# Optimization experiments

Measured on AMD Instinct MI355X. Metric: run time of the kernel, lower is better.

The kernel has to match this reference:

```python
import jax, jax.numpy as jnp
import numpy as np

NU, NI, F, H, D = 100000, 50000, 256, 8, 64
E1, E2 = 300000, 300000
SLOPE = 0.2  # DGL GATConv default negative_slope


def setup_inputs() -> dict:
    key = jax.random.key(0)
    ks = jax.random.split(key, 20)
    p = lambda k, sh: jax.random.normal(k, sh, jnp.float32) * 0.1
    return {
        "h_user": jax.random.normal(ks[0], (NU, F), jnp.float32),
        "h_item": jax.random.normal(ks[1], (NI, F), jnp.float32),
        "src_u2i": jax.random.randint(ks[2], (E1,), 0, NU),
        "dst_u2i": jax.random.randint(ks[3], (E1,), 0, NI),
        "src_i2u": jax.random.randint(ks[4], (E2,), 0, NI),
        "dst_i2u": jax.random.randint(ks[5], (E2,), 0, NU),
        "W_src_u2i": p(ks[6], (F, H * D)), "W_dst_u2i": p(ks[7], (F, H * D)),
        "al_u2i": p(ks[8], (H, D)), "ar_u2i": p(ks[9], (H, D)),
        "bias_u2i": jnp.zeros((H * D,), jnp.float32), "W_res_u2i": p(ks[10], (F, H * D)),
        "W_src_i2u": p(ks[11], (F, H * D)), "W_dst_i2u": p(ks[12], (F, H * D)),
        "al_i2u": p(ks[13], (H, D)), "ar_i2u": p(ks[14], (H, D)),
        "bias_i2u": jnp.zeros((H * D,), jnp.float32), "W_res_i2u": p(ks[15], (F, H * D)),
    }


def _gat(h_src, h_dst, src, dst, Ws, Wd, al, ar, b, Wr, n_dst):
    # linear projections -> [N, H, D]
    fs = (h_src @ Ws).reshape(-1, H, D)
    fd = (h_dst @ Wd).reshape(-1, H, D)
    el = jnp.einsum('nhd,hd->nh', fs, al)   # a_l . Wh_src
    er = jnp.einsum('nhd,hd->nh', fd, ar)   # a_r . Wh_dst
    e = jax.nn.leaky_relu(el[src] + er[dst], SLOPE)  # [E, H]
    # segment softmax over incoming edges of each dst node
    m = jax.ops.segment_max(e, dst, num_segments=n_dst)
    m = jnp.where(jnp.isfinite(m), m, jnp.float32(0))  # nodes with no edges
    ex = jnp.exp(e - m[dst])
    s = jax.ops.segment_sum(ex, dst, num_segments=n_dst)
    a = ex / s[dst]                                   # [E, H]
    # weighted scatter-sum of gathered source features
    out = jax.ops.segment_sum(a[:, :, None] * fs[src], dst, num_segments=n_dst)
    res = (h_dst @ Wr).reshape(-1, H, D)              # residual projection
    return out + res + b.reshape(1, H, D)


def reference(h_user, h_item, src_u2i, dst_u2i, src_i2u, dst_i2u,
              W_src_u2i, W_dst_u2i, al_u2i, ar_u2i, bias_u2i, W_res_u2i,
              W_src_i2u, W_dst_i2u, al_i2u, ar_i2u, bias_i2u, W_res_i2u):
    out_item = _gat(h_user, h_item, src_u2i, dst_u2i,
                    W_src_u2i, W_dst_u2i, al_u2i, ar_u2i, bias_u2i, W_res_u2i, NI)
    out_user = _gat(h_item, h_user, src_i2u, dst_i2u,
                    W_src_i2u, W_dst_i2u, al_i2u, ar_i2u, bias_i2u, W_res_i2u, NU)
    return (out_user, out_item)
```

## Files before the change

kernel.cpp:

```cpp
#include <hip/hip_runtime.h>
#include <cstdint>
#include <cstddef>

#define NU_ 100000
#define NI_ 50000
#define F_ 256
#define H_ 8
#define HD_ 512
#define NE_ 300000
#define SLOPE_ 0.2f

#define MPAD_U 100096
#define MPAD_I 50048
#define MT_U (MPAD_U / 128)
#define MT_I (MPAD_I / 128)
#define GEMM_NB ((MT_U + MT_I) * 4)

#define SCAN_N (NI_ + NU_)
#define SCAN_CHUNK 2048
#define SCAN_NB ((SCAN_N + SCAN_CHUNK - 1) / SCAN_CHUNK)

#define PREP_COPY_U (NU_ * F_ / 2048)
#define PREP_COPY_I (NI_ * F_ / 2048)
#define PREP_COPY (PREP_COPY_U + PREP_COPY_I)
#define PREP_WCONV 2048
#define PREP_FOLD 32
#define PREP_HIST ((2 * NE_ + 255) / 256)
#define PREP_NB (PREP_COPY + PREP_WCONV + PREP_FOLD + PREP_HIST)

typedef float f32x4 __attribute__((ext_vector_type(4)));
typedef __bf16 bf16x8 __attribute__((ext_vector_type(8)));
typedef unsigned short u16x8 __attribute__((ext_vector_type(8)));
typedef unsigned short u16x4 __attribute__((ext_vector_type(4)));

static __device__ __forceinline__ unsigned short f2bf_bits(float f) {
  unsigned u = __float_as_uint(f);
  u += 0x7fffu + ((u >> 16) & 1u);
  return (unsigned short)(u >> 16);
}
static __device__ __forceinline__ float bf2f(unsigned short b) {
  return __uint_as_float(((unsigned)b) << 16);
}

#define GLL16(g, l)                                                        \
  __builtin_amdgcn_global_load_lds(                                        \
      (const __attribute__((address_space(1))) void*)(g),                  \
      (__attribute__((address_space(3))) void*)(l), 16, 0, 0)

__global__ __launch_bounds__(256) void prep_kernel(const float* __restrict__ h_user,
                                                   const float* __restrict__ h_item,
                                                   const float* __restrict__ W0,
                                                   const float* __restrict__ W1,
                                                   const float* __restrict__ W2,
                                                   const float* __restrict__ W3,
                                                   const float* __restrict__ Wd0,
                                                   const float* __restrict__ Wd1,
                                                   const float* __restrict__ a0,
                                                   const float* __restrict__ a1,
                                                   const float* __restrict__ a2,
                                                   const float* __restrict__ a3,
                                                   const int* __restrict__ dst_u2i,
                                                   const int* __restrict__ dst_i2u,
                                                   unsigned short* __restrict__ hb_user,
                                                   unsigned short* __restrict__ hb_item,
                                                   unsigned short* __restrict__ Wt,
                                                   unsigned short* __restrict__ wfb,
                                                   int* __restrict__ deg) {
  int bid = blockIdx.x;
  if (bid < PREP_COPY) {
    bool user = bid < PREP_COPY_U;
    const float* h = user ? h_user : h_item;
    unsigned short* hb = user ? hb_user : hb_item;
    size_t base = (size_t)(user ? bid : bid - PREP_COPY_U) * 2048 + threadIdx.x * 8;
    f32x4 a = *(const f32x4*)&h[base];
    f32x4 b = *(const f32x4*)&h[base + 4];
    u16x8 o;
    o[0] = f2bf_bits(a.x); o[1] = f2bf_bits(a.y); o[2] = f2bf_bits(a.z); o[3] = f2bf_bits(a.w);
    o[4] = f2bf_bits(b.x); o[5] = f2bf_bits(b.y); o[6] = f2bf_bits(b.z); o[7] = f2bf_bits(b.w);
    *(u16x8*)&hb[base] = o;
  } else if (bid < PREP_COPY + PREP_WCONV) {
    int idx = (bid - PREP_COPY) * 256 + threadIdx.x;
    int m = idx >> 17;
    int r = idx & 131071;
    const float* W = (m == 0) ? W0 : (m == 1) ? W1 : (m == 2) ? W2 : W3;
    int f = r & 255, c = r >> 8;
    Wt[idx] = f2bf_bits(W[(size_t)f * HD_ + c]);
  } else if (bid < PREP_COPY + PREP_WCONV + PREP_FOLD) {
    int b = bid - PREP_COPY - PREP_WCONV;
    int m = b >> 3;
    int idx = (b & 7) * 256 + threadIdx.x;
    const float* W = (m == 0) ? W0 : (m == 1) ? Wd0 : (m == 2) ? W2 : Wd1;
    const float* av = (m == 0) ? a0 : (m == 1) ? a1 : (m == 2) ? a2 : a3;
    int f = idx & 255, hh = idx >> 8;
    float acc = 0.f;
#pragma unroll 8
    for (int d = 0; d < 64; ++d) acc += W[(size_t)f * HD_ + hh * 64 + d] * av[hh * 64 + d];
    int buf = (m == 0 || m == 3) ? 0 : 1;
    int rowoff = (m == 1 || m == 3) ? 8 : 0;
    wfb[buf * 4096 + (rowoff + hh) * 256 + f] = f2bf_bits(acc);
  } else {
    int e = (bid - PREP_COPY - PREP_WCONV - PREP_FOLD) * 256 + threadIdx.x;
    if (e < NE_) atomicAdd(&deg[dst_u2i[e]], 1);
    else if (e < 2 * NE_) atomicAdd(&deg[NI_ + dst_i2u[e - NE_]], 1);
  }
}

__global__ __launch_bounds__(256) void gemm2_kernel(const unsigned short* __restrict__ hb_user,
                                                    const unsigned short* __restrict__ hb_item,
                                                    const unsigned short* __restrict__ Wt,
                                                    const unsigned short* __restrict__ wfb,
                                                    unsigned short* __restrict__ fs_u2i,
                                                    unsigned short* __restrict__ fs_i2u,
                                                    unsigned short* __restrict__ res_user,
                                                    unsigned short* __restrict__ res_item,
                                                    const float* __restrict__ bias_u2i,
                                                    const float* __restrict__ bias_i2u,
                                                    float* __restrict__ el_u2i,
                                                    float* __restrict__ er_i2u,
                                                    float* __restrict__ el_i2u,
                                                    float* __restrict__ er_u2i,
                                                    const int* __restrict__ deg,
                                                    int* __restrict__ bsum) {
  __shared__ unsigned short lds[2][3][128][32];
  __shared__ unsigned short wflds[2][16][32];
  if (blockIdx.x >= GEMM_NB) {
    int* ilds = (int*)&lds[0][0][0][0];
    int tid = threadIdx.x;
    int base = (blockIdx.x - GEMM_NB) * SCAN_CHUNK + tid * 8;
    int sum = 0;
#pragma unroll
    for (int j = 0; j < 8; ++j) sum += (base + j < SCAN_N) ? deg[base + j] : 0;
    ilds[tid] = sum;
    __syncthreads();
    for (int o = 128; o > 0; o >>= 1) {
      if (tid < o) ilds[tid] += ilds[tid + o];
      __syncthreads();
    }
    if (tid == 0) bsum[blockIdx.x - GEMM_NB] = ilds[0];
    return;
  }
  int bid;
  {
    constexpr int qq = GEMM_NB / 8, rr = GEMM_NB % 8;
    int xcd = blockIdx.x & 7, sidx = blockIdx.x >> 3;
    bid = (xcd < rr ? xcd * (qq + 1) : rr * (qq + 1) + (xcd - rr) * qq) + sidx;
  }
  bool user = bid < MT_U * 4;
  if (!user) bid -= MT_U * 4;
  const unsigned short* Ab  = user ? hb_user : hb_item;
  const unsigned short* B1t = user ? (Wt + 0 * HD_ * F_) : (Wt + 2 * HD_ * F_);
  const unsigned short* B2t = user ? (Wt + 3 * HD_ * F_) : (Wt + 1 * HD_ * F_);
  const unsigned short* wfs = user ? wfb : (wfb + 4096);
  unsigned short* fs  = user ? fs_u2i : fs_i2u;
  unsigned short* res = user ? res_user : res_item;
  const float* bias = user ? bias_i2u : bias_u2i;
  int M = user ? NU_ : NI_;

  int tid = threadIdx.x;
  int lane = tid & 63;
  int wave = tid >> 6;
  int wm = wave >> 1, wn = wave & 1;
  int mt = bid >> 2, nt = bid & 3;
  int bm = mt * 128, bn = nt * 128;
  f32x4 acc1[4][4] = {};
  f32x4 acc2[4][4] = {};
  f32x4 acc3[4] = {};
  int lr = lane & 15;
  int ksw = ((lane >> 4) ^ ((lr >> 1) & 3)) << 3;

  int r0 = tid >> 2;
  int c0 = (tid & 3) << 3;
  int cs = (((tid & 3) ^ ((r0 >> 1) & 3)) << 3);
  const unsigned short* gA  = &Ab [(size_t)(bm + r0) * 256 + cs];
  const unsigned short* gB1 = &B1t[(size_t)(bn + r0) * 256 + cs];
  const unsigned short* gB2 = &B2t[(size_t)(bn + r0) * 256 + cs];
  const unsigned short* gW  = &wfs[(size_t)(tid >> 2) * 256 + cs];

#define STAGE(buf, t)                                                       \
  do {                                                                      \
    int k0_ = (t) * 32;                                                     \
    GLL16(gA  + k0_,          &lds[buf][0][r0][c0]);                        \
    GLL16(gA  + k0_ + 64*256, &lds[buf][0][r0 + 64][c0]);                   \
    GLL16(gB1 + k0_,          &lds[buf][1][r0][c0]);                        \
    GLL16(gB1 + k0_ + 64*256, &lds[buf][1][r0 + 64][c0]);                   \
    GLL16(gB2 + k0_,          &lds[buf][2][r0][c0]);                        \
    GLL16(gB2 + k0_ + 64*256, &lds[buf][2][r0 + 64][c0]);                   \
    if (nt == 0 && tid < 64) GLL16(gW + k0_, &wflds[buf][tid >> 2][c0]);    \
  } while (0)

  STAGE(0, 0);
#pragma unroll
  for (int t = 0; t < 8; ++t) {
    if (t < 7) STAGE((t + 1) & 1, t + 1);
    if (t < 7) asm volatile("s_waitcnt vmcnt(6)" ::: "memory");
    else       asm volatile("s_waitcnt vmcnt(0)" ::: "memory");
    __builtin_amdgcn_s_barrier();
    __builtin_amdgcn_sched_barrier(0);
    const int cb = t & 1;
    bf16x8 af[4], b1[4], b2[4];
#pragma unroll
    for (int m = 0; m < 4; ++m)
      af[m] = __builtin_bit_cast(bf16x8, *(const u16x8*)&lds[cb][0][wm * 64 + m * 16 + lr][ksw]);
#pragma unroll
    for (int n = 0; n < 4; ++n) {
      b1[n] = __builtin_bit_cast(bf16x8, *(const u16x8*)&lds[cb][1][wn * 64 + n * 16 + lr][ksw]);
      b2[n] = __builtin_bit_cast(bf16x8, *(const u16x8*)&lds[cb][2][wn * 64 + n * 16 + lr][ksw]);
    }
#pragma unroll
    for (int m = 0; m < 4; ++m)
#pragma unroll
      for (int n = 0; n < 4; ++n) {
        acc1[m][n] = __builtin_amdgcn_mfma_f32_16x16x32_bf16(af[m], b1[n], acc1[m][n], 0, 0, 0);
        acc2[m][n] = __builtin_amdgcn_mfma_f32_16x16x32_bf16(af[m], b2[n], acc2[m][n], 0, 0, 0);
      }
    if (nt == 0) {
      bf16x8 b3 = __builtin_bit_cast(bf16x8, *(const u16x8*)&wflds[cb][lr][ksw]);
#pragma unroll
      for (int m = 0; m < 4; ++m)
        acc3[m] = __builtin_amdgcn_mfma_f32_16x16x32_bf16(af[m], b3, acc3[m], 0, 0, 0);
    }
    __builtin_amdgcn_sched_barrier(0);
    __builtin_amdgcn_s_barrier();
  }
#undef STAGE

  int rg = (lane >> 4) * 4;
#pragma unroll
  for (int m = 0; m < 4; ++m) {
#pragma unroll
    for (int r = 0; r < 4; ++r) {
      int row = bm + wm * 64 + m * 16 + rg + r;
      if (row >= M) continue;
#pragma unroll
      for (int n = 0; n < 4; ++n) {
        int col = bn + wn * 64 + n * 16 + lr;
        fs[(size_t)row * HD_ + col]  = f2bf_bits(acc1[m][n][r]);
        res[(size_t)row * HD_ + col] = f2bf_bits(acc2[m][n][r] + bias[col]);
      }
    }
  }
  if (nt == 0 && wn == 0) {
    float* elp = user ? el_u2i : el_i2u;
    float* erp = user ? er_i2u : er_u2i;
#pragma unroll
    for (int m = 0; m < 4; ++m) {
#pragma unroll
      for (int r = 0; r < 4; ++r) {
        int row = bm + wm * 64 + m * 16 + rg + r;
        if (row >= M) continue;
        if (lr < 8) elp[(size_t)row * 8 + lr] = acc3[m][r];
        else        erp[(size_t)row * 8 + lr - 8] = acc3[m][r];
      }
    }
  }
}

__global__ __launch_bounds__(256) void scan_apply_kernel(const int* __restrict__ deg,
                                                         const int* __restrict__ bsum,
                                                         int* __restrict__ rowstart,
                                                         int* __restrict__ cursor) {
  __shared__ int sb[128];
  __shared__ int lds[256];
  int tid = threadIdx.x;
  if (tid < 128) sb[tid] = (tid < SCAN_NB) ? bsum[tid] : 0;
  __syncthreads();
  for (int o = 1; o < 128; o <<= 1) {
    int t = (tid < 128 && tid >= o) ? sb[tid - o] : 0;
    __syncthreads();
    if (tid < 128) sb[tid] += t;
    __syncthreads();
  }
  int blockpref = (blockIdx.x == 0) ? 0 : sb[blockIdx.x - 1];
  int base = blockIdx.x * SCAN_CHUNK + tid * 8;
  int v[8];
  int sum = 0;
#pragma unroll
  for (int j = 0; j < 8; ++j) {
    v[j] = (base + j < SCAN_N) ? deg[base + j] : 0;
    sum += v[j];
  }
  lds[tid] = sum;
  __syncthreads();
  for (int o = 1; o < 256; o <<= 1) {
    int t = (tid >= o) ? lds[tid - o] : 0;
    __syncthreads();
    lds[tid] += t;
    __syncthreads();
  }
  int run = blockpref + lds[tid] - sum;
#pragma unroll
  for (int j = 0; j < 8; ++j) {
    if (base + j < SCAN_N) { rowstart[base + j] = run; cursor[base + j] = run; }
    run += v[j];
  }
  if (blockIdx.x == 0 && tid == 0) rowstart[SCAN_N] = 2 * NE_;
}

__global__ __launch_bounds__(256) void bin_kernel(const int* __restrict__ src_u2i,
                                                  const int* __restrict__ dst_u2i,
                                                  const int* __restrict__ src_i2u,
                                                  const int* __restrict__ dst_i2u,
                                                  int* __restrict__ cursor,
                                                  int* __restrict__ ssrc) {
  int e = blockIdx.x * 256 + threadIdx.x;
  int de, se;
  if (e < NE_) { de = dst_u2i[e]; se = src_u2i[e]; }
  else if (e < 2 * NE_) { de = NI_ + dst_i2u[e - NE_]; se = src_i2u[e - NE_]; }
  else return;
  int pos = atomicAdd(&cursor[de], 1);
  ssrc[pos] = se;
}

__global__ __launch_bounds__(256) void accum_kernel(const int* __restrict__ rowstart,
                                                    const int* __restrict__ ssrc,
                                                    const float* __restrict__ el_u2i,
                                                    const float* __restrict__ el_i2u,
                                                    const float* __restrict__ er_u2i,
                                                    const float* __restrict__ er_i2u,
                                                    const unsigned short* __restrict__ fs_u2i,
                                                    const unsigned short* __restrict__ fs_i2u,
                                                    const unsigned short* __restrict__ res_user,
                                                    const unsigned short* __restrict__ res_item,
                                                    float* __restrict__ out_item,
                                                    float* __restrict__ out_user) {
  int n = blockIdx.x * 4 + (threadIdx.x >> 6);
  int lane = threadIdx.x & 63;
  bool item = n < NI_;
  int ln = item ? n : n - NI_;
  const unsigned short* res = item ? res_item : res_user;
  float* out = (item ? out_item : out_user) + (size_t)ln * HD_;
  int r0 = rowstart[n], r1 = rowstart[n + 1];
  float acc[8] = {};
  if (r0 < r1) {
    const float* el = item ? el_u2i : el_i2u;
    const float* er = item ? er_u2i : er_i2u;
    const unsigned short* fs = item ? fs_u2i : fs_i2u;
    int hh = lane >> 3;
    float erh = er[(size_t)ln * 8 + hh];
    float m = -3.0e38f, s = 0.f;
    int k = r0;
    for (; k + 2 <= r1; k += 2) {
      int s0 = ssrc[k], s1 = ssrc[k + 1];
      float e0 = el[(size_t)s0 * 8 + hh] + erh;
      float e1 = el[(size_t)s1 * 8 + hh] + erh;
      e0 = e0 > 0.f ? e0 : SLOPE_ * e0;
      e1 = e1 > 0.f ? e1 : SLOPE_ * e1;
      u16x8 v0 = *(const u16x8*)&fs[(size_t)s0 * HD_ + lane * 8];
      u16x8 v1 = *(const u16x8*)&fs[(size_t)s1 * HD_ + lane * 8];
      float mm = fmaxf(e0, e1);
      if (mm > m) {
        float r = __expf(m - mm);
        s *= r;
#pragma unroll
        for (int j = 0; j < 8; ++j) acc[j] *= r;
        m = mm;
      }
      float x0 = __expf(e0 - m), x1 = __expf(e1 - m);
      s += x0 + x1;
#pragma unroll
      for (int j = 0; j < 8; ++j)
        acc[j] += x0 * bf2f((unsigned short)v0[j]) + x1 * bf2f((unsigned short)v1[j]);
    }
    if (k < r1) {
      int s0 = ssrc[k];
      float e0 = el[(size_t)s0 * 8 + hh] + erh;
      e0 = e0 > 0.f ? e0 : SLOPE_ * e0;
      u16x8 v0 = *(const u16x8*)&fs[(size_t)s0 * HD_ + lane * 8];
      if (e0 > m) {
        float r = __expf(m - e0);
        s *= r;
#pragma unroll
        for (int j = 0; j < 8; ++j) acc[j] *= r;
        m = e0;
      }
      float x0 = __expf(e0 - m);
      s += x0;
#pragma unroll
      for (int j = 0; j < 8; ++j) acc[j] += x0 * bf2f((unsigned short)v0[j]);
    }
    float inv = 1.f / s;
#pragma unroll
    for (int j = 0; j < 8; ++j) acc[j] *= inv;
  }
  u16x8 rv = *(const u16x8*)&res[(size_t)ln * HD_ + lane * 8];
  f32x4 o0, o1;
#pragma unroll
  for (int j = 0; j < 4; ++j) {
    o0[j] = acc[j] + bf2f((unsigned short)rv[j]);
    o1[j] = acc[4 + j] + bf2f((unsigned short)rv[4 + j]);
  }
  float* op = out + lane * 8;
  *(f32x4*)op = o0;
  *(f32x4*)(op + 4) = o1;
}

extern "C" void kernel_launch(void* const* d_in, const int* in_sizes, int n_in,
                              void* d_out, int out_size, void* d_ws, size_t ws_size,
                              hipStream_t stream) {
  const float* h_user    = (const float*)d_in[0];
  const float* h_item    = (const float*)d_in[1];
  const int*   src_u2i   = (const int*)d_in[2];
  const int*   dst_u2i   = (const int*)d_in[3];
  const int*   src_i2u   = (const int*)d_in[4];
  const int*   dst_i2u   = (const int*)d_in[5];
  const float* W_src_u2i = (const float*)d_in[6];
  const float* W_dst_u2i = (const float*)d_in[7];
  const float* al_u2i    = (const float*)d_in[8];
  const float* ar_u2i    = (const float*)d_in[9];
  const float* bias_u2i  = (const float*)d_in[10];
  const float* W_res_u2i = (const float*)d_in[11];
  const float* W_src_i2u = (const float*)d_in[12];
  const float* W_dst_i2u = (const float*)d_in[13];
  const float* al_i2u    = (const float*)d_in[14];
  const float* ar_i2u    = (const float*)d_in[15];
  const float* bias_i2u  = (const float*)d_in[16];
  const float* W_res_i2u = (const float*)d_in[17];

  float* out_user = (float*)d_out;
  float* out_item = (float*)d_out + (size_t)NU_ * HD_;

  char* ws = (char*)d_ws;
  size_t off = 0;
  auto take = [&](size_t bytes) -> char* {
    char* p = ws + off;
    off += (bytes + 255) & ~(size_t)255;
    return p;
  };
  unsigned short* fs_u2i   = (unsigned short*)take((size_t)NU_ * HD_ * 2);
  unsigned short* fs_i2u   = (unsigned short*)take((size_t)NI_ * HD_ * 2);
  unsigned short* res_user = (unsigned short*)take((size_t)NU_ * HD_ * 2);
  unsigned short* res_item = (unsigned short*)take((size_t)NI_ * HD_ * 2);
  unsigned short* hb_user  = (unsigned short*)take((size_t)MPAD_U * F_ * 2);
  unsigned short* hb_item  = (unsigned short*)take((size_t)MPAD_I * F_ * 2);
  unsigned short* Wt  = (unsigned short*)take((size_t)4 * HD_ * F_ * 2);
  unsigned short* wfb = (unsigned short*)take((size_t)2 * 16 * F_ * 2);
  float* el_u2i = (float*)take((size_t)NU_ * 8 * 4);
  float* er_i2u = (float*)take((size_t)NU_ * 8 * 4);
  float* el_i2u = (float*)take((size_t)NI_ * 8 * 4);
  float* er_u2i = (float*)take((size_t)NI_ * 8 * 4);
  int* deg_all      = (int*)take((size_t)SCAN_N * 4);
  int* rowstart_all = (int*)take((size_t)(SCAN_N + 1) * 4);
  int* cursor_all   = (int*)take((size_t)SCAN_N * 4);
  int* bsum         = (int*)take((size_t)128 * 4);
  int* ssrc         = (int*)take((size_t)2 * NE_ * 4);

  hipMemsetAsync(deg_all, 0, (size_t)SCAN_N * 4, stream);

  prep_kernel<<<PREP_NB, 256, 0, stream>>>(h_user, h_item,
                                           W_src_u2i, W_res_u2i, W_src_i2u, W_res_i2u,
                                           W_dst_u2i, W_dst_i2u,
                                           al_u2i, ar_u2i, al_i2u, ar_i2u,
                                           dst_u2i, dst_i2u,
                                           hb_user, hb_item, Wt, wfb, deg_all);

  gemm2_kernel<<<GEMM_NB + SCAN_NB, 256, 0, stream>>>(hb_user, hb_item, Wt, wfb,
                                                      fs_u2i, fs_i2u, res_user, res_item,
                                                      bias_u2i, bias_i2u,
                                                      el_u2i, er_i2u, el_i2u, er_u2i,
                                                      deg_all, bsum);

  scan_apply_kernel<<<SCAN_NB, 256, 0, stream>>>(deg_all, bsum, rowstart_all, cursor_all);
  constexpr int EB2 = (2 * NE_ + 255) / 256;
  bin_kernel<<<EB2, 256, 0, stream>>>(src_u2i, dst_u2i, src_i2u, dst_i2u, cursor_all, ssrc);

  accum_kernel<<<SCAN_N / 4, 256, 0, stream>>>(rowstart_all, ssrc,
                                               el_u2i, el_i2u, er_u2i, er_i2u,
                                               fs_u2i, fs_i2u, res_user, res_item,
                                               out_item, out_user);
}
```

Before: 502.0 us.

## Load GEMM operands directly from global memory instead of LDS double-buffering

Removes the global_load_lds double-buffered staging and barriers in the fused projection GEMM. Each wave now loads its MFMA A/B fragments straight from global memory (bf16x8 per lane), relying on L1/L2 for reuse. Launch bounds now request two blocks per SM. This removes LDS traffic and synchronisation, but operands shared across waves are fetched redundantly, so the kernel leans on cache bandwidth and load latency.

```diff
diff --git a/kernel.cpp b/kernel.cpp
--- a/kernel.cpp
+++ b/kernel.cpp
@@ -41,11 +41,6 @@
 static __device__ __forceinline__ float bf2f(unsigned short b) {
   return __uint_as_float(((unsigned)b) << 16);
 }
-
-#define GLL16(g, l)                                                        \
-  __builtin_amdgcn_global_load_lds(                                        \
-      (const __attribute__((address_space(1))) void*)(g),                  \
-      (__attribute__((address_space(3))) void*)(l), 16, 0, 0)
 
 __global__ __launch_bounds__(256) void prep_kernel(const float* __restrict__ h_user,
                                                    const float* __restrict__ h_item,
@@ -105,26 +100,24 @@
   }
 }
 
-__global__ __launch_bounds__(256) void gemm2_kernel(const unsigned short* __restrict__ hb_user,
-                                                    const unsigned short* __restrict__ hb_item,
-                                                    const unsigned short* __restrict__ Wt,
-                                                    const unsigned short* __restrict__ wfb,
-                                                    unsigned short* __restrict__ fs_u2i,
-                                                    unsigned short* __restrict__ fs_i2u,
-                                                    unsigned short* __restrict__ res_user,
-                                                    unsigned short* __restrict__ res_item,
-                                                    const float* __restrict__ bias_u2i,
-                                                    const float* __restrict__ bias_i2u,
-                                                    float* __restrict__ el_u2i,
-                                                    float* __restrict__ er_i2u,
-                                                    float* __restrict__ el_i2u,
-                                                    float* __restrict__ er_u2i,
-                                                    const int* __restrict__ deg,
-                                                    int* __restrict__ bsum) {
-  __shared__ unsigned short lds[2][3][128][32];
-  __shared__ unsigned short wflds[2][16][32];
+__global__ __launch_bounds__(256, 2) void gemm2_kernel(const unsigned short* __restrict__ hb_user,
+                                                       const unsigned short* __restrict__ hb_item,
+                                                       const unsigned short* __restrict__ Wt,
+                                                       const unsigned short* __restrict__ wfb,
+                                                       unsigned short* __restrict__ fs_u2i,
+                                                       unsigned short* __restrict__ fs_i2u,
+                                                       unsigned short* __restrict__ res_user,
+                                                       unsigned short* __restrict__ res_item,
+                                                       const float* __restrict__ bias_u2i,
+                                                       const float* __restrict__ bias_i2u,
+                                                       float* __restrict__ el_u2i,
+                                                       float* __restrict__ er_i2u,
+                                                       float* __restrict__ el_i2u,
+                                                       float* __restrict__ er_u2i,
+                                                       const int* __restrict__ deg,
+                                                       int* __restrict__ bsum) {
+  __shared__ int ilds[256];
   if (blockIdx.x >= GEMM_NB) {
-    int* ilds = (int*)&lds[0][0][0][0];
     int tid = threadIdx.x;
     int base = (blockIdx.x - GEMM_NB) * SCAN_CHUNK + tid * 8;
     int sum = 0;
@@ -166,45 +159,24 @@
   f32x4 acc2[4][4] = {};
   f32x4 acc3[4] = {};
   int lr = lane & 15;
-  int ksw = ((lane >> 4) ^ ((lr >> 1) & 3)) << 3;
-
-  int r0 = tid >> 2;
-  int c0 = (tid & 3) << 3;
-  int cs = (((tid & 3) ^ ((r0 >> 1) & 3)) << 3);
-  const unsigned short* gA  = &Ab [(size_t)(bm + r0) * 256 + cs];
-  const unsigned short* gB1 = &B1t[(size_t)(bn + r0) * 256 + cs];
-  const unsigned short* gB2 = &B2t[(size_t)(bn + r0) * 256 + cs];
-  const unsigned short* gW  = &wfs[(size_t)(tid >> 2) * 256 + cs];
-
-#define STAGE(buf, t)                                                       \
-  do {                                                                      \
-    int k0_ = (t) * 32;                                                     \
-    GLL16(gA  + k0_,          &lds[buf][0][r0][c0]);                        \
-    GLL16(gA  + k0_ + 64*256, &lds[buf][0][r0 + 64][c0]);                   \
-    GLL16(gB1 + k0_,          &lds[buf][1][r0][c0]);                        \
-    GLL16(gB1 + k0_ + 64*256, &lds[buf][1][r0 + 64][c0]);                   \
-    GLL16(gB2 + k0_,          &lds[buf][2][r0][c0]);                        \
-    GLL16(gB2 + k0_ + 64*256, &lds[buf][2][r0 + 64][c0]);                   \
-    if (nt == 0 && tid < 64) GLL16(gW + k0_, &wflds[buf][tid >> 2][c0]);    \
-  } while (0)
-
-  STAGE(0, 0);
+  int kk = (lane >> 4) * 8;
+
+  const unsigned short* pA0 = &Ab [(size_t)(bm + wm * 64 + lr) * 256 + kk];
+  const unsigned short* pB1 = &B1t[(size_t)(bn + wn * 64 + lr) * 256 + kk];
+  const unsigned short* pB2 = &B2t[(size_t)(bn + wn * 64 + lr) * 256 + kk];
+  const unsigned short* pW  = &wfs[(size_t)lr * 256 + kk];
+
 #pragma unroll
   for (int t = 0; t < 8; ++t) {
-    if (t < 7) STAGE((t + 1) & 1, t + 1);
-    if (t < 7) asm volatile("s_waitcnt vmcnt(6)" ::: "memory");
-    else       asm volatile("s_waitcnt vmcnt(0)" ::: "memory");
-    __builtin_amdgcn_s_barrier();
-    __builtin_amdgcn_sched_barrier(0);
-    const int cb = t & 1;
+    const int ko = t * 32;
     bf16x8 af[4], b1[4], b2[4];
 #pragma unroll
     for (int m = 0; m < 4; ++m)
-      af[m] = __builtin_bit_cast(bf16x8, *(const u16x8*)&lds[cb][0][wm * 64 + m * 16 + lr][ksw]);
+      af[m] = __builtin_bit_cast(bf16x8, *(const u16x8*)(pA0 + (size_t)m * 16 * 256 + ko));
 #pragma unroll
     for (int n = 0; n < 4; ++n) {
-      b1[n] = __builtin_bit_cast(bf16x8, *(const u16x8*)&lds[cb][1][wn * 64 + n * 16 + lr][ksw]);
-      b2[n] = __builtin_bit_cast(bf16x8, *(const u16x8*)&lds[cb][2][wn * 64 + n * 16 + lr][ksw]);
+      b1[n] = __builtin_bit_cast(bf16x8, *(const u16x8*)(pB1 + (size_t)n * 16 * 256 + ko));
+      b2[n] = __builtin_bit_cast(bf16x8, *(const u16x8*)(pB2 + (size_t)n * 16 * 256 + ko));
     }
 #pragma unroll
     for (int m = 0; m < 4; ++m)
@@ -214,15 +186,12 @@
         acc2[m][n] = __builtin_amdgcn_mfma_f32_16x16x32_bf16(af[m], b2[n], acc2[m][n], 0, 0, 0);
       }
     if (nt == 0) {
-      bf16x8 b3 = __builtin_bit_cast(bf16x8, *(const u16x8*)&wflds[cb][lr][ksw]);
+      bf16x8 b3 = __builtin_bit_cast(bf16x8, *(const u16x8*)(pW + ko));
 #pragma unroll
       for (int m = 0; m < 4; ++m)
         acc3[m] = __builtin_amdgcn_mfma_f32_16x16x32_bf16(af[m], b3, acc3[m], 0, 0, 0);
     }
-    __builtin_amdgcn_sched_barrier(0);
-    __builtin_amdgcn_s_barrier();
-  }
-#undef STAGE
+  }
 
   int rg = (lane >> 4) * 4;
 #pragma unroll
```

Result: slower. 565.1 us (+12.6%).

## Make GEMM kernel persistent with cross-tile prefetch and fused scan partials

Applied to the files above, without the earlier changes.

Converts the projection GEMM into a persistent kernel of 768 blocks. Each block loops over its XCD-local tiles and prefetches the next tile's first K-slice while it finishes the current one. The block-sum scan work moves onto the first blocks, ahead of their GEMM tiles, and the attention-weight operand is read directly from global memory instead of being staged in LDS. It also sets launch bounds for three blocks per CU. The aim is to cut launch and tail overhead and hide pipeline fill between tiles, at the cost of possible register pressure and uncached global reads for the el/er operand.

```diff
diff --git a/kernel.cpp b/kernel.cpp
--- a/kernel.cpp
+++ b/kernel.cpp
@@ -15,6 +15,8 @@
 #define MT_U (MPAD_U / 128)
 #define MT_I (MPAD_I / 128)
 #define GEMM_NB ((MT_U + MT_I) * 4)
+#define GEMM_BLOCKS 768
+#define GEMM_LB 96
 
 #define SCAN_N (NI_ + NU_)
 #define SCAN_CHUNK 2048
@@ -105,28 +107,28 @@
   }
 }
 
-__global__ __launch_bounds__(256) void gemm2_kernel(const unsigned short* __restrict__ hb_user,
-                                                    const unsigned short* __restrict__ hb_item,
-                                                    const unsigned short* __restrict__ Wt,
-                                                    const unsigned short* __restrict__ wfb,
-                                                    unsigned short* __restrict__ fs_u2i,
-                                                    unsigned short* __restrict__ fs_i2u,
-                                                    unsigned short* __restrict__ res_user,
-                                                    unsigned short* __restrict__ res_item,
-                                                    const float* __restrict__ bias_u2i,
-                                                    const float* __restrict__ bias_i2u,
-                                                    float* __restrict__ el_u2i,
-                                                    float* __restrict__ er_i2u,
-                                                    float* __restrict__ el_i2u,
-                                                    float* __restrict__ er_u2i,
-                                                    const int* __restrict__ deg,
-                                                    int* __restrict__ bsum) {
+__global__ __launch_bounds__(256, 3) void gemm2_kernel(const unsigned short* __restrict__ hb_user,
+                                                       const unsigned short* __restrict__ hb_item,
+                                                       const unsigned short* __restrict__ Wt,
+                                                       const unsigned short* __restrict__ wfb,
+                                                       unsigned short* __restrict__ fs_u2i,
+                                                       unsigned short* __restrict__ fs_i2u,
+                                                       unsigned short* __restrict__ res_user,
+                                                       unsigned short* __restrict__ res_item,
+                                                       const float* __restrict__ bias_u2i,
+                                                       const float* __restrict__ bias_i2u,
+                                                       float* __restrict__ el_u2i,
+                                                       float* __restrict__ er_i2u,
+                                                       float* __restrict__ el_i2u,
+                                                       float* __restrict__ er_u2i,
+                                                       const int* __restrict__ deg,
+                                                       int* __restrict__ bsum) {
   __shared__ unsigned short lds[2][3][128][32];
-  __shared__ unsigned short wflds[2][16][32];
-  if (blockIdx.x >= GEMM_NB) {
+  int tid = threadIdx.x;
+
+  if (blockIdx.x < SCAN_NB) {
     int* ilds = (int*)&lds[0][0][0][0];
-    int tid = threadIdx.x;
-    int base = (blockIdx.x - GEMM_NB) * SCAN_CHUNK + tid * 8;
+    int base = blockIdx.x * SCAN_CHUNK + tid * 8;
     int sum = 0;
 #pragma unroll
     for (int j = 0; j < 8; ++j) sum += (base + j < SCAN_N) ? deg[base + j] : 0;
@@ -136,123 +138,146 @@
       if (tid < o) ilds[tid] += ilds[tid + o];
       __syncthreads();
     }
-    if (tid == 0) bsum[blockIdx.x - GEMM_NB] = ilds[0];
-    return;
-  }
-  int bid;
-  {
-    constexpr int qq = GEMM_NB / 8, rr = GEMM_NB % 8;
-    int xcd = blockIdx.x & 7, sidx = blockIdx.x >> 3;
-    bid = (xcd < rr ? xcd * (qq + 1) : rr * (qq + 1) + (xcd - rr) * qq) + sidx;
-  }
-  bool user = bid < MT_U * 4;
-  if (!user) bid -= MT_U * 4;
-  const unsigned short* Ab  = user ? hb_user : hb_item;
-  const unsigned short* B1t = user ? (Wt + 0 * HD_ * F_) : (Wt + 2 * HD_ * F_);
-  const unsigned short* B2t = user ? (Wt + 3 * HD_ * F_) : (Wt + 1 * HD_ * F_);
-  const unsigned short* wfs = user ? wfb : (wfb + 4096);
-  unsigned short* fs  = user ? fs_u2i : fs_i2u;
-  unsigned short* res = user ? res_user : res_item;
-  const float* bias = user ? bias_i2u : bias_u2i;
-  int M = user ? NU_ : NI_;
-
-  int tid = threadIdx.x;
+    if (tid == 0) bsum[blockIdx.x] = ilds[0];
+    __syncthreads();
+  }
+
   int lane = tid & 63;
   int wave = tid >> 6;
   int wm = wave >> 1, wn = wave & 1;
-  int mt = bid >> 2, nt = bid & 3;
-  int bm = mt * 128, bn = nt * 128;
-  f32x4 acc1[4][4] = {};
-  f32x4 acc2[4][4] = {};
-  f32x4 acc3[4] = {};
   int lr = lane & 15;
+  int kk = (lane >> 4) * 8;
   int ksw = ((lane >> 4) ^ ((lr >> 1) & 3)) << 3;
-
   int r0 = tid >> 2;
   int c0 = (tid & 3) << 3;
-  int cs = (((tid & 3) ^ ((r0 >> 1) & 3)) << 3);
-  const unsigned short* gA  = &Ab [(size_t)(bm + r0) * 256 + cs];
-  const unsigned short* gB1 = &B1t[(size_t)(bn + r0) * 256 + cs];
-  const unsigned short* gB2 = &B2t[(size_t)(bn + r0) * 256 + cs];
-  const unsigned short* gW  = &wfs[(size_t)(tid >> 2) * 256 + cs];
-
-#define STAGE(buf, t)                                                       \
+  int csofs = (((tid & 3) ^ ((r0 >> 1) & 3)) << 3);
+
+  int xcd = blockIdx.x & 7;
+  int lb = blockIdx.x >> 3;
+  constexpr int qq = GEMM_NB / 8, rr = GEMM_NB % 8;
+  int tbeg = (xcd < rr) ? xcd * (qq + 1) : rr * (qq + 1) + (xcd - rr) * qq;
+  int tend = tbeg + qq + (xcd < rr ? 1 : 0);
+
+  const unsigned short *gA, *gB1, *gB2;
+  auto setup = [&](int tl) {
+    int b = tl;
+    bool us = b < MT_U * 4;
+    if (!us) b -= MT_U * 4;
+    const unsigned short* Ab = us ? hb_user : hb_item;
+    const unsigned short* B1 = us ? (Wt + 0 * HD_ * F_) : (Wt + 2 * HD_ * F_);
+    const unsigned short* B2 = us ? (Wt + 3 * HD_ * F_) : (Wt + 1 * HD_ * F_);
+    int mt = b >> 2, nt = b & 3;
+    gA  = &Ab[(size_t)(mt * 128 + r0) * 256 + csofs];
+    gB1 = &B1[(size_t)(nt * 128 + r0) * 256 + csofs];
+    gB2 = &B2[(size_t)(nt * 128 + r0) * 256 + csofs];
+  };
+
+#define STAGE6(buf, k0_)                                                    \
   do {                                                                      \
-    int k0_ = (t) * 32;                                                     \
-    GLL16(gA  + k0_,          &lds[buf][0][r0][c0]);                        \
-    GLL16(gA  + k0_ + 64*256, &lds[buf][0][r0 + 64][c0]);                   \
-    GLL16(gB1 + k0_,          &lds[buf][1][r0][c0]);                        \
-    GLL16(gB1 + k0_ + 64*256, &lds[buf][1][r0 + 64][c0]);                   \
-    GLL16(gB2 + k0_,          &lds[buf][2][r0][c0]);                        \
-    GLL16(gB2 + k0_ + 64*256, &lds[buf][2][r0 + 64][c0]);                   \
-    if (nt == 0 && tid < 64) GLL16(gW + k0_, &wflds[buf][tid >> 2][c0]);    \
+    GLL16(gA  + (k0_),            &lds[buf][0][r0][c0]);                    \
+    GLL16(gA  + (k0_) + 64 * 256, &lds[buf][0][r0 + 64][c0]);               \
+    GLL16(gB1 + (k0_),            &lds[buf][1][r0][c0]);                    \
+    GLL16(gB1 + (k0_) + 64 * 256, &lds[buf][1][r0 + 64][c0]);               \
+    GLL16(gB2 + (k0_),            &lds[buf][2][r0][c0]);                    \
+    GLL16(gB2 + (k0_) + 64 * 256, &lds[buf][2][r0 + 64][c0]);               \
   } while (0)
 
-  STAGE(0, 0);
-#pragma unroll
-  for (int t = 0; t < 8; ++t) {
-    if (t < 7) STAGE((t + 1) & 1, t + 1);
-    if (t < 7) asm volatile("s_waitcnt vmcnt(6)" ::: "memory");
-    else       asm volatile("s_waitcnt vmcnt(0)" ::: "memory");
-    __builtin_amdgcn_s_barrier();
-    __builtin_amdgcn_sched_barrier(0);
-    const int cb = t & 1;
-    bf16x8 af[4], b1[4], b2[4];
-#pragma unroll
-    for (int m = 0; m < 4; ++m)
-      af[m] = __builtin_bit_cast(bf16x8, *(const u16x8*)&lds[cb][0][wm * 64 + m * 16 + lr][ksw]);
-#pragma unroll
-    for (int n = 0; n < 4; ++n) {
-      b1[n] = __builtin_bit_cast(bf16x8, *(const u16x8*)&lds[cb][1][wn * 64 + n * 16 + lr][ksw]);
-      b2[n] = __builtin_bit_cast(bf16x8, *(const u16x8*)&lds[cb][2][wn * 64 + n * 16 + lr][ksw]);
-    }
-#pragma unroll
-    for (int m = 0; m < 4; ++m)
+  int tl = tbeg + lb;
+  if (tl >= tend) return;
+  setup(tl);
+  STAGE6(0, 0);
+
+  for (; tl < tend; tl += GEMM_LB) {
+    int b = tl;
+    bool user = b < MT_U * 4;
+    if (!user) b -= MT_U * 4;
+    int mt = b >> 2, nt = b & 3;
+    int bm = mt * 128, bn = nt * 128;
+    unsigned short* fs  = user ? fs_u2i : fs_i2u;
+    unsigned short* res = user ? res_user : res_item;
+    const float* bias = user ? bias_i2u : bias_u2i;
+    const unsigned short* wfs = user ? wfb : (wfb + 4096);
+    int M = user ? NU_ : NI_;
+    int nextl = tl + GEMM_LB;
+    bool havenext = nextl < tend;
+
+    f32x4 acc1[4][4] = {};
+    f32x4 acc2[4][4] = {};
+    f32x4 acc3[4] = {};
+
+#pragma unroll
+    for (int t = 0; t < 8; ++t) {
+      bool staged = true;
+      if (t < 7) {
+        STAGE6((t + 1) & 1, (t + 1) * 32);
+      } else if (havenext) {
+        setup(nextl);
+        STAGE6(0, 0);
+      } else {
+        staged = false;
+      }
+      if (staged) asm volatile("s_waitcnt vmcnt(6)" ::: "memory");
+      else        asm volatile("s_waitcnt vmcnt(0)" ::: "memory");
+      __builtin_amdgcn_s_barrier();
+      __builtin_amdgcn_sched_barrier(0);
+      const int cb = t & 1;
+      bf16x8 af[4], b1[4], b2[4];
+#pragma unroll
+      for (int m = 0; m < 4; ++m)
+        af[m] = __builtin_bit_cast(bf16x8, *(const u16x8*)&lds[cb][0][wm * 64 + m * 16 + lr][ksw]);
 #pragma unroll
       for (int n = 0; n < 4; ++n) {
-        acc1[m][n] = __builtin_amdgcn_mfma_f32_16x16x32_bf16(af[m], b1[n], acc1[m][n], 0, 0, 0);
-        acc2[m][n] = __builtin_amdgcn_mfma_f32_16x16x32_bf16(af[m], b2[n], acc2[m][n], 0, 0, 0);
-      }
-    if (nt == 0) {
-      bf16x8 b3 = __builtin_bit_cast(bf16x8, *(const u16x8*)&wflds[cb][lr][ksw]);
+        b1[n] = __builtin_bit_cast(bf16x8, *(const u16x8*)&lds[cb][1][wn * 64 + n * 16 + lr][ksw]);
+        b2[n] = __builtin_bit_cast(bf16x8, *(const u16x8*)&lds[cb][2][wn * 64 + n * 16 + lr][ksw]);
+      }
 #pragma unroll
       for (int m = 0; m < 4; ++m)
-        acc3[m] = __builtin_amdgcn_mfma_f32_16x16x32_bf16(af[m], b3, acc3[m], 0, 0, 0);
-    }
-    __builtin_amdgcn_sched_barrier(0);
-    __builtin_amdgcn_s_barrier();
-  }
-#undef STAGE
-
-  int rg = (lane >> 4) * 4;
-#pragma unroll
-  for (int m = 0; m < 4; ++m) {
-#pragma unroll
-    for (int r = 0; r < 4; ++r) {
-      int row = bm + wm * 64 + m * 16 + rg + r;
-      if (row >= M) continue;
-#pragma unroll
-      for (int n = 0; n < 4; ++n) {
-        int col = bn + wn * 64 + n * 16 + lr;
-        fs[(size_t)row * HD_ + col]  = f2bf_bits(acc1[m][n][r]);
-        res[(size_t)row * HD_ + col] = f2bf_bits(acc2[m][n][r] + bias[col]);
-      }
-    }
-  }
-  if (nt == 0 && wn == 0) {
-    float* elp = user ? el_u2i : el_i2u;
-    float* erp = user ? er_i2u : er_u2i;
+#pragma unroll
+        for (int n = 0; n < 4; ++n) {
+          acc1[m][n] = __builtin_amdgcn_mfma_f32_16x16x32_bf16(af[m], b1[n], acc1[m][n], 0, 0, 0);
+          acc2[m][n] = __builtin_amdgcn_mfma_f32_16x16x32_bf16(af[m], b2[n], acc2[m][n], 0, 0, 0);
+        }
+      if (nt == 0) {
+        bf16x8 b3 = __builtin_bit_cast(bf16x8, *(const u16x8*)&wfs[(size_t)lr * 256 + kk + t * 32]);
+#pragma unroll
+        for (int m = 0; m < 4; ++m)
+          acc3[m] = __builtin_amdgcn_mfma_f32_16x16x32_bf16(af[m], b3, acc3[m], 0, 0, 0);
+      }
+      __builtin_amdgcn_sched_barrier(0);
+      __builtin_amdgcn_s_barrier();
+    }
+
+    int rg = (lane >> 4) * 4;
 #pragma unroll
     for (int m = 0; m < 4; ++m) {
 #pragma unroll
       for (int r = 0; r < 4; ++r) {
         int row = bm + wm * 64 + m * 16 + rg + r;
         if (row >= M) continue;
-        if (lr < 8) elp[(size_t)row * 8 + lr] = acc3[m][r];
-        else        erp[(size_t)row * 8 + lr - 8] = acc3[m][r];
-      }
-    }
-  }
+#pragma unroll
+        for (int n = 0; n < 4; ++n) {
+          int col = bn + wn * 64 + n * 16 + lr;
+          fs[(size_t)row * HD_ + col]  = f2bf_bits(acc1[m][n][r]);
+          res[(size_t)row * HD_ + col] = f2bf_bits(acc2[m][n][r] + bias[col]);
+        }
+      }
+    }
+    if (nt == 0 && wn == 0) {
+      float* elp = user ? el_u2i : el_i2u;
+      float* erp = user ? er_i2u : er_u2i;
+#pragma unroll
+      for (int m = 0; m < 4; ++m) {
+#pragma unroll
+        for (int r = 0; r < 4; ++r) {
+          int row = bm + wm * 64 + m * 16 + rg + r;
+          if (row >= M) continue;
+          if (lr < 8) elp[(size_t)row * 8 + lr] = acc3[m][r];
+          else        erp[(size_t)row * 8 + lr - 8] = acc3[m][r];
+        }
+      }
+    }
+  }
+#undef STAGE6
 }
 
 __global__ __launch_bounds__(256) void scan_apply_kernel(const int* __restrict__ deg,
@@ -453,11 +478,11 @@
                                            dst_u2i, dst_i2u,
                                            hb_user, hb_item, Wt, wfb, deg_all);
 
-  gemm2_kernel<<<GEMM_NB + SCAN_NB, 256, 0, stream>>>(hb_user, hb_item, Wt, wfb,
-                                                      fs_u2i, fs_i2u, res_user, res_item,
-                                                      bias_u2i, bias_i2u,
-                                                      el_u2i, er_i2u, el_i2u, er_u2i,
-                                                      deg_all, bsum);
+  gemm2_kernel<<<GEMM_BLOCKS, 256, 0, stream>>>(hb_user, hb_item, Wt, wfb,
+                                                fs_u2i, fs_i2u, res_user, res_item,
+                                                bias_u2i, bias_i2u,
+                                                el_u2i, er_i2u, el_i2u, er_u2i,
+                                                deg_all, bsum);
 
   scan_apply_kernel<<<SCAN_NB, 256, 0, stream>>>(deg_all, bsum, rowstart_all, cursor_all);
   constexpr int EB2 = (2 * NE_ + 255) / 256;
```

New measurement: 670.0 us. +33.5%, slower.

## Hold attention-fold weights in registers and vectorize transposed bf16 epilogue stores

Applied to the files above, without the earlier changes.

The small attention-fold weight tile is now loaded once into registers per block instead of being staged through LDS each k-step, which removes one async copy and one LDS read per iteration. The MFMA operands are swapped so each lane holds four consecutive columns. That lets the epilogue pack them with v_cvt_pk_bf16_f32 and write 8-byte vector stores instead of scalar 2-byte stores, with the bias loaded as a float4. The cost is higher register pressure from the eight held weight fragments, and the B-fragment register load reads an unswizzled global layout whose correctness depends on the weight layout.

```diff
diff --git a/kernel.cpp b/kernel.cpp
--- a/kernel.cpp
+++ b/kernel.cpp
@@ -40,6 +40,11 @@
 }
 static __device__ __forceinline__ float bf2f(unsigned short b) {
   return __uint_as_float(((unsigned)b) << 16);
+}
+static __device__ __forceinline__ unsigned cvt_pk_bf16(float lo, float hi) {
+  unsigned r;
+  asm("v_cvt_pk_bf16_f32 %0, %1, %2" : "=v"(r) : "v"(lo), "v"(hi));
+  return r;
 }
 
 #define GLL16(g, l)                                                        \
@@ -122,7 +127,6 @@
                                                     const int* __restrict__ deg,
                                                     int* __restrict__ bsum) {
   __shared__ unsigned short lds[2][3][128][32];
-  __shared__ unsigned short wflds[2][16][32];
   if (blockIdx.x >= GEMM_NB) {
     int* ilds = (int*)&lds[0][0][0][0];
     int tid = threadIdx.x;
@@ -166,6 +170,7 @@
   f32x4 acc2[4][4] = {};
   f32x4 acc3[4] = {};
   int lr = lane & 15;
+  int kk = (lane >> 4) * 8;
   int ksw = ((lane >> 4) ^ ((lr >> 1) & 3)) << 3;
 
   int r0 = tid >> 2;
@@ -174,7 +179,13 @@
   const unsigned short* gA  = &Ab [(size_t)(bm + r0) * 256 + cs];
   const unsigned short* gB1 = &B1t[(size_t)(bn + r0) * 256 + cs];
   const unsigned short* gB2 = &B2t[(size_t)(bn + r0) * 256 + cs];
-  const unsigned short* gW  = &wfs[(size_t)(tid >> 2) * 256 + cs];
+
+  bf16x8 b3f[8];
+  if (nt == 0) {
+#pragma unroll
+    for (int t = 0; t < 8; ++t)
+      b3f[t] = __builtin_bit_cast(bf16x8, *(const u16x8*)&wfs[(size_t)lr * 256 + kk + t * 32]);
+  }
 
 #define STAGE(buf, t)                                                       \
   do {                                                                      \
@@ -185,7 +196,6 @@
     GLL16(gB1 + k0_ + 64*256, &lds[buf][1][r0 + 64][c0]);                   \
     GLL16(gB2 + k0_,          &lds[buf][2][r0][c0]);                        \
     GLL16(gB2 + k0_ + 64*256, &lds[buf][2][r0 + 64][c0]);                   \
-    if (nt == 0 && tid < 64) GLL16(gW + k0_, &wflds[buf][tid >> 2][c0]);    \
   } while (0)
 
   STAGE(0, 0);
@@ -210,14 +220,13 @@
     for (int m = 0; m < 4; ++m)
 #pragma unroll
       for (int n = 0; n < 4; ++n) {
-        acc1[m][n] = __builtin_amdgcn_mfma_f32_16x16x32_bf16(af[m], b1[n], acc1[m][n], 0, 0, 0);
-        acc2[m][n] = __builtin_amdgcn_mfma_f32_16x16x32_bf16(af[m], b2[n], acc2[m][n], 0, 0, 0);
+        acc1[m][n] = __builtin_amdgcn_mfma_f32_16x16x32_bf16(b1[n], af[m], acc1[m][n], 0, 0, 0);
+        acc2[m][n] = __builtin_amdgcn_mfma_f32_16x16x32_bf16(b2[n], af[m], acc2[m][n], 0, 0, 0);
       }
     if (nt == 0) {
-      bf16x8 b3 = __builtin_bit_cast(bf16x8, *(const u16x8*)&wflds[cb][lr][ksw]);
 #pragma unroll
       for (int m = 0; m < 4; ++m)
-        acc3[m] = __builtin_amdgcn_mfma_f32_16x16x32_bf16(af[m], b3, acc3[m], 0, 0, 0);
+        acc3[m] = __builtin_amdgcn_mfma_f32_16x16x32_bf16(af[m], b3f[t], acc3[m], 0, 0, 0);
     }
     __builtin_amdgcn_sched_barrier(0);
     __builtin_amdgcn_s_barrier();
@@ -225,17 +234,25 @@
 #undef STAGE
 
   int rg = (lane >> 4) * 4;
+  f32x4 bsv[4];
+#pragma unroll
+  for (int n = 0; n < 4; ++n)
+    bsv[n] = *(const f32x4*)&bias[bn + wn * 64 + n * 16 + rg];
 #pragma unroll
   for (int m = 0; m < 4; ++m) {
-#pragma unroll
-    for (int r = 0; r < 4; ++r) {
-      int row = bm + wm * 64 + m * 16 + rg + r;
-      if (row >= M) continue;
+    int row = bm + wm * 64 + m * 16 + lr;
+    if (row < M) {
 #pragma unroll
       for (int n = 0; n < 4; ++n) {
-        int col = bn + wn * 64 + n * 16 + lr;
-        fs[(size_t)row * HD_ + col]  = f2bf_bits(acc1[m][n][r]);
-        res[(size_t)row * HD_ + col] = f2bf_bits(acc2[m][n][r] + bias[col]);
+        int col = bn + wn * 64 + n * 16 + rg;
+        uint2 v1;
+        v1.x = cvt_pk_bf16(acc1[m][n][0], acc1[m][n][1]);
+        v1.y = cvt_pk_bf16(acc1[m][n][2], acc1[m][n][3]);
+        *(uint2*)&fs[(size_t)row * HD_ + col] = v1;
+        uint2 v2;
+        v2.x = cvt_pk_bf16(acc2[m][n][0] + bsv[n].x, acc2[m][n][1] + bsv[n].y);
+        v2.y = cvt_pk_bf16(acc2[m][n][2] + bsv[n].z, acc2[m][n][3] + bsv[n].w);
+        *(uint2*)&res[(size_t)row * HD_ + col] = v2;
       }
     }
   }
```

Result: no change. 498.0 us (-0.8%).
